# Kernel optimization log

Hardware: AMD Instinct MI355X
Metric: run time of the kernel (lower is better)

The kernel has to match this reference:

```python
import jax, jax.numpy as jnp
import numpy as np

B, T, D = 32, 512, 1024
N = 65536
H, L = 150, 17


def setup_inputs() -> dict:
    key = jax.random.key(0)
    ks = jax.random.split(key, 5)
    xs = jax.random.normal(ks[0], (B, T, D), dtype=jnp.float32)
    spans = jax.random.randint(ks[1], (N, 2), 0, T, dtype=jnp.int64 if jax.config.jax_enable_x64 else jnp.int32)
    batch_ids = jax.random.randint(ks[2], (N,), 0, B, dtype=spans.dtype)
    W1 = jax.random.normal(ks[3], (2 * D, H), dtype=jnp.float32) / np.sqrt(2 * D)
    b1 = jnp.zeros((H,), dtype=jnp.float32)
    W2 = jax.random.normal(ks[4], (H, L), dtype=jnp.float32) / np.sqrt(H)
    b2 = jnp.zeros((L,), dtype=jnp.float32)
    return {"xs": xs, "spans": spans, "batch_ids": batch_ids,
            "W1": W1, "b1": b1, "W2": W2, "b2": b2}


def reference(xs, spans, batch_ids, W1, b1, W2, b2):
    # Flatten batch/time: xs_flat [B*T, D]; offset span indices into flat space,
    # mirroring `idxs + max_length * i` in the torch forward.
    d = xs.shape[-1]
    xs_flat = xs.reshape(-1, d)
    flat_idx = spans + batch_ids[:, None] * xs.shape[1]  # [N, 2]
    # feature == 'concat': gather begin/end token reps and concat -> [N, 2D]
    feats = xs_flat[flat_idx.reshape(-1)].reshape(flat_idx.shape[0], 2 * d)
    h = jax.nn.relu(feats @ W1 + b1)  # MLP hidden layer (dropout p=0)
    scores = h @ W2 + b2              # output layer, no activation
    return scores  # [N, num_labels]; torch.split is a zero-copy view, omitted
```

## Files before the change

kernel.cpp:

```cpp
#include <hip/hip_runtime.h>
#include <stdint.h>

#define TT 512
#define DD 1024
#define NN 65536
#define HH 150
#define LL 17

typedef __bf16 bf16_t;
typedef short shortx8 __attribute__((ext_vector_type(8)));
typedef short shortx4 __attribute__((ext_vector_type(4)));
typedef float f32x4 __attribute__((ext_vector_type(4)));

typedef __attribute__((address_space(1))) const void gconst_void;
typedef __attribute__((address_space(3))) void lds_void;

static __device__ __forceinline__ short f2bf(float f) {
  return (short)__builtin_bit_cast(unsigned short, (bf16_t)f);
}
static __device__ __forceinline__ float bf2f(short s) {
  unsigned u = ((unsigned)(unsigned short)s) << 16;
  return __builtin_bit_cast(float, u);
}

__global__ __launch_bounds__(256) void prep_w(
    const float* __restrict__ W1, const float* __restrict__ W2,
    short* __restrict__ Bpp, short* __restrict__ W2p)
{
  int task = blockIdx.x * 256 + threadIdx.x;
  const int NW1 = 32 * 20 * 64;
  if (task < NW1) {
    int kb  = task / 1280;
    int rem = task - kb * 1280;
    int cb = rem >> 6, l = rem & 63;
    int cc   = cb * 16 + (l & 15);
    int half = (cc >= 160) ? 1 : 0;
    int hc   = cc - 160 * half;
    int krow = half * 1024 + kb * 32 + (l >> 4) * 8;
    shortx8 v;
#pragma unroll
    for (int j = 0; j < 8; ++j) {
      float f = (hc < HH) ? W1[(krow + j) * HH + hc] : 0.f;
      v[j] = f2bf(f);
    }
    *reinterpret_cast<shortx8*>(Bpp + task * 8) = v;
  } else if (task < NW1 + 640) {
    int t2 = task - NW1;
    int kb  = t2 >> 7;
    int rem = t2 & 127;
    int cb = rem >> 6, l = rem & 63;
    int col  = cb * 16 + (l & 15);
    int krow = kb * 32 + (l >> 4) * 8;
    shortx8 v;
#pragma unroll
    for (int j = 0; j < 8; ++j) {
      int r = krow + j;
      float f = (r < HH && col < LL) ? W2[r * LL + col] : 0.f;
      v[j] = f2bf(f);
    }
    *reinterpret_cast<shortx8*>(W2p + t2 * 8) = v;
  }
}

__global__ __launch_bounds__(512, 2) void k1_gemm(
    const float* __restrict__ xs, const short* __restrict__ Bpp,
    const float* __restrict__ b1, short* __restrict__ H)
{
  __shared__ __align__(16) char lds[81920];

  const int tid  = threadIdx.x;
  const int wv   = tid >> 6;
  const int wr   = wv >> 2;
  const int wc   = wv & 3;
  const int lane = tid & 63;
  const int l15  = lane & 15;
  const int kg   = lane >> 4;
  const int blk  = blockIdx.x;

  const char* ab[2];
#pragma unroll
  for (int rfi = 0; rfi < 2; ++rfi) {
    int row = blk * 64 + wr * 32 + rfi * 16 + l15;
    ab[rfi] = (const char*)xs + (size_t)row * 4096;
  }

  f32x4 acc[2][5];
  {
    f32x4 z = {0.f, 0.f, 0.f, 0.f};
#pragma unroll
    for (int rfi = 0; rfi < 2; ++rfi)
#pragma unroll
      for (int cbl = 0; cbl < 5; ++cbl) acc[rfi][cbl] = z;
  }

  shortx8 xbA[2][2], xbB[2][2];

#define STAGE(c, p) do { _Pragma("unroll") \
    for (int i = 0; i < 5; ++i) { \
      int f_ = wv * 5 + i;                      \
      int s_ = f_ / 20, cbb_ = f_ % 20; \
      const char* g_ = (const char*)Bpp + \
          (size_t)(((2 * (c) + s_) * 20 + cbb_) * 64 + lane) * 16; \
      char* l_ = lds + (p) * 40960 + f_ * 1024; \
      __builtin_amdgcn_global_load_lds((gconst_void*)g_, (lds_void*)l_, 16, 0, 0); \
    } \
  } while (0)

#define LOADX(c, xb) do { _Pragma("unroll") \
    for (int rfi = 0; rfi < 2; ++rfi) \
      _Pragma("unroll") \
      for (int s = 0; s < 2; ++s) { \
        int off_ = (2 * (c) + s) * 128 + kg * 32; \
        f32x4 x_ = *reinterpret_cast<const f32x4*>(ab[rfi] + off_); \
        f32x4 y_ = *reinterpret_cast<const f32x4*>(ab[rfi] + off_ + 16); \
        shortx8 t_; \
        t_[0]=f2bf(x_[0]); t_[1]=f2bf(x_[1]); t_[2]=f2bf(x_[2]); t_[3]=f2bf(x_[3]); \
        t_[4]=f2bf(y_[0]); t_[5]=f2bf(y_[1]); t_[6]=f2bf(y_[2]); t_[7]=f2bf(y_[3]); \
        xb[rfi][s] = t_; \
      } \
  } while (0)

#define COMP(p, xb) do { _Pragma("unroll") \
    for (int s = 0; s < 2; ++s) { \
      shortx8 w1f[5]; \
      _Pragma("unroll") \
      for (int cbl = 0; cbl < 5; ++cbl) \
        w1f[cbl] = *reinterpret_cast<const shortx8*>( \
            lds + (p) * 40960 + (s * 20 + wc * 5 + cbl) * 1024 + lane * 16); \
      _Pragma("unroll") \
      for (int rfi = 0; rfi < 2; ++rfi) \
        _Pragma("unroll") \
        for (int cbl = 0; cbl < 5; ++cbl) \
          acc[rfi][cbl] = __builtin_amdgcn_mfma_f32_16x16x32_bf16( \
              w1f[cbl], xb[rfi][s], acc[rfi][cbl], 0, 0, 0); \
    } \
  } while (0)

#define WAITBAR() do { \
    asm volatile("s_waitcnt vmcnt(8)" ::: "memory"); \
    __builtin_amdgcn_s_barrier(); \
    __builtin_amdgcn_sched_barrier(0); \
  } while (0)

  STAGE(0, 0);
  LOADX(0, xbA);
  WAITBAR();

  for (int cp = 0; cp < 8; ++cp) {
    int c0 = 2 * cp;
    STAGE(c0 + 1, 1);
    LOADX(c0 + 1, xbB);
    COMP(0, xbA);
    WAITBAR();
    if (cp < 7) {
      STAGE(c0 + 2, 0);
      LOADX(c0 + 2, xbA);
    }
    COMP(1, xbB);
    if (cp < 7) WAITBAR();
  }
#undef STAGE
#undef LOADX
#undef COMP
#undef WAITBAR

#pragma unroll
  for (int cbl = 0; cbl < 5; ++cbl) {
    int c0 = wc * 80 + cbl * 16 + kg * 4;
    f32x4 badd;
#pragma unroll
    for (int i = 0; i < 4; ++i)
      badd[i] = (c0 + i < HH) ? b1[c0 + i] : 0.f;
#pragma unroll
    for (int rfi = 0; rfi < 2; ++rfi) {
      f32x4 v = acc[rfi][cbl] + badd;
      shortx4 hv;
      hv[0] = f2bf(v[0]); hv[1] = f2bf(v[1]); hv[2] = f2bf(v[2]); hv[3] = f2bf(v[3]);
      int hrow = blk * 64 + wr * 32 + rfi * 16 + l15;
      *reinterpret_cast<shortx4*>(H + (size_t)hrow * 320 + c0) = hv;
    }
  }
}

__global__ __launch_bounds__(256, 4) void k2_span(
    const int* __restrict__ spans, const int* __restrict__ bids,
    const short* __restrict__ H, const short* __restrict__ W2p,
    const float* __restrict__ b2, float* __restrict__ out)
{
  const int tid  = threadIdx.x;
  const int wv   = tid >> 6;
  const int lane = tid & 63;
  const int l15  = lane & 15;
  const int kg   = lane >> 4;
  const int blk  = blockIdx.x;

  shortx8 wf[5][2];
#pragma unroll
  for (int ks = 0; ks < 5; ++ks)
#pragma unroll
    for (int cb2 = 0; cb2 < 2; ++cb2)
      wf[ks][cb2] = *reinterpret_cast<const shortx8*>(
          W2p + ((ks * 2 + cb2) * 64 + lane) * 8);

  int r  = blk * 64 + wv * 16 + l15;
  int bb = bids[r];
  int rb = bb * TT + spans[2 * r + 0];
  int re = bb * TT + spans[2 * r + 1];
  const short* pa = H + (size_t)rb * 320;
  const short* pb = H + (size_t)re * 320 + 160;

  shortx8 af[5];
#pragma unroll
  for (int ks = 0; ks < 5; ++ks) {
    shortx8 ha = *reinterpret_cast<const shortx8*>(pa + ks * 32 + kg * 8);
    shortx8 hb = *reinterpret_cast<const shortx8*>(pb + ks * 32 + kg * 8);
    shortx8 t;
#pragma unroll
    for (int j = 0; j < 8; ++j) {
      float f = bf2f(ha[j]) + bf2f(hb[j]);
      t[j] = f2bf(fmaxf(f, 0.f));
    }
    af[ks] = t;
  }

  f32x4 acc2[2];
  {
    f32x4 z = {0.f, 0.f, 0.f, 0.f};
    acc2[0] = z; acc2[1] = z;
  }
#pragma unroll
  for (int ks = 0; ks < 5; ++ks)
#pragma unroll
    for (int cb2 = 0; cb2 < 2; ++cb2)
      acc2[cb2] = __builtin_amdgcn_mfma_f32_16x16x32_bf16(
          af[ks], wf[ks][cb2], acc2[cb2], 0, 0, 0);

#pragma unroll
  for (int cb2 = 0; cb2 < 2; ++cb2) {
    int col = cb2 * 16 + l15;
    if (col < LL) {
      float bv = b2[col];
#pragma unroll
      for (int i = 0; i < 4; ++i) {
        int row = blk * 64 + wv * 16 + kg * 4 + i;
        out[(size_t)row * LL + col] = acc2[cb2][i] + bv;
      }
    }
  }
}

extern "C" void kernel_launch(void* const* d_in, const int* in_sizes, int n_in,
                              void* d_out, int out_size, void* d_ws, size_t ws_size,
                              hipStream_t stream) {
  const float* xs    = (const float*)d_in[0];
  const int*   spans = (const int*)d_in[1];
  const int*   bids  = (const int*)d_in[2];
  const float* W1    = (const float*)d_in[3];
  const float* b1    = (const float*)d_in[4];
  const float* W2    = (const float*)d_in[5];
  const float* b2    = (const float*)d_in[6];
  float* out = (float*)d_out;

  short* H   = (short*)d_ws;
  short* Bpp = H + 16384 * 320;
  short* W2p = Bpp + 327680;

  prep_w<<<163, 256, 0, stream>>>(W1, W2, Bpp, W2p);
  k1_gemm<<<256, 512, 0, stream>>>(xs, Bpp, b1, H);
  k2_span<<<1024, 256, 0, stream>>>(spans, bids, H, W2p, b2, out);
}
```

Measured before the change: 148.7 us.

## Stage activations in swizzled LDS and stream W1 fragments via registers

```diff
diff --git a/kernel.cpp b/kernel.cpp
--- a/kernel.cpp
+++ b/kernel.cpp
@@ -11,9 +11,6 @@
 typedef short shortx8 __attribute__((ext_vector_type(8)));
 typedef short shortx4 __attribute__((ext_vector_type(4)));
 typedef float f32x4 __attribute__((ext_vector_type(4)));
-
-typedef __attribute__((address_space(1))) const void gconst_void;
-typedef __attribute__((address_space(3))) void lds_void;
 
 static __device__ __forceinline__ short f2bf(float f) {
   return (short)__builtin_bit_cast(unsigned short, (bf16_t)f);
@@ -62,107 +59,116 @@
   }
 }
 
-__global__ __launch_bounds__(512, 2) void k1_gemm(
+__global__ __launch_bounds__(256, 1) void k1_gemm(
     const float* __restrict__ xs, const short* __restrict__ Bpp,
     const float* __restrict__ b1, short* __restrict__ H)
 {
-  __shared__ __align__(16) char lds[81920];
+  __shared__ __align__(16) char lds[16384];
 
   const int tid  = threadIdx.x;
-  const int wv   = tid >> 6;
-  const int wr   = wv >> 2;
-  const int wc   = wv & 3;
+  const int wc   = tid >> 6;
   const int lane = tid & 63;
   const int l15  = lane & 15;
   const int kg   = lane >> 4;
   const int blk  = blockIdx.x;
 
-  const char* ab[2];
-#pragma unroll
-  for (int rfi = 0; rfi < 2; ++rfi) {
-    int row = blk * 64 + wr * 32 + rfi * 16 + l15;
-    ab[rfi] = (const char*)xs + (size_t)row * 4096;
-  }
-
-  f32x4 acc[2][5];
+  const int arow = tid >> 2;
+  const int acol = (tid & 3) * 16;
+  const float* ag = xs + (size_t)(blk * 64 + arow) * 1024 + acol;
+  const int awb = arow * 128 + (tid & 3) * 32;
+  const int aswz_w = (arow & 7) << 4;
+  const int arb = l15 * 128 + kg * 16;
+  const int aswz_r = (l15 & 7) << 4;
+
+  const shortx8* bg = reinterpret_cast<const shortx8*>(Bpp) + (size_t)wc * 5 * 64;
+
+  f32x4 acc[4][5];
   {
     f32x4 z = {0.f, 0.f, 0.f, 0.f};
 #pragma unroll
-    for (int rfi = 0; rfi < 2; ++rfi)
-#pragma unroll
-      for (int cbl = 0; cbl < 5; ++cbl) acc[rfi][cbl] = z;
-  }
-
-  shortx8 xbA[2][2], xbB[2][2];
-
-#define STAGE(c, p) do { _Pragma("unroll") \
-    for (int i = 0; i < 5; ++i) { \
-      int f_ = wv * 5 + i;                      \
-      int s_ = f_ / 20, cbb_ = f_ % 20; \
-      const char* g_ = (const char*)Bpp + \
-          (size_t)(((2 * (c) + s_) * 20 + cbb_) * 64 + lane) * 16; \
-      char* l_ = lds + (p) * 40960 + f_ * 1024; \
-      __builtin_amdgcn_global_load_lds((gconst_void*)g_, (lds_void*)l_, 16, 0, 0); \
-    } \
-  } while (0)
-
-#define LOADX(c, xb) do { _Pragma("unroll") \
-    for (int rfi = 0; rfi < 2; ++rfi) \
-      _Pragma("unroll") \
-      for (int s = 0; s < 2; ++s) { \
-        int off_ = (2 * (c) + s) * 128 + kg * 32; \
-        f32x4 x_ = *reinterpret_cast<const f32x4*>(ab[rfi] + off_); \
-        f32x4 y_ = *reinterpret_cast<const f32x4*>(ab[rfi] + off_ + 16); \
-        shortx8 t_; \
-        t_[0]=f2bf(x_[0]); t_[1]=f2bf(x_[1]); t_[2]=f2bf(x_[2]); t_[3]=f2bf(x_[3]); \
-        t_[4]=f2bf(y_[0]); t_[5]=f2bf(y_[1]); t_[6]=f2bf(y_[2]); t_[7]=f2bf(y_[3]); \
-        xb[rfi][s] = t_; \
-      } \
-  } while (0)
-
-#define COMP(p, xb) do { _Pragma("unroll") \
-    for (int s = 0; s < 2; ++s) { \
-      shortx8 w1f[5]; \
+    for (int rf = 0; rf < 4; ++rf)
+#pragma unroll
+      for (int cbl = 0; cbl < 5; ++cbl) acc[rf][cbl] = z;
+  }
+
+  f32x4 aregA[4], aregB[4];
+  shortx8 bregA[10], bregB[10];
+
+#define GLOAD_A(reg, c) do { _Pragma("unroll") \
+    for (int i = 0; i < 4; ++i) \
+      reg[i] = *reinterpret_cast<const f32x4*>(ag + (c) * 64 + i * 4); \
+  } while (0)
+
+#define GLOAD_B(reg, c) do { _Pragma("unroll") \
+    for (int s = 0; s < 2; ++s) \
       _Pragma("unroll") \
       for (int cbl = 0; cbl < 5; ++cbl) \
-        w1f[cbl] = *reinterpret_cast<const shortx8*>( \
-            lds + (p) * 40960 + (s * 20 + wc * 5 + cbl) * 1024 + lane * 16); \
+        reg[s * 5 + cbl] = bg[(size_t)((2 * (c) + s) * 20 + cbl) * 64 + lane]; \
+  } while (0)
+
+#define WRITE_A(reg, p) do { \
+    shortx8 lo_, hi_; \
+    _Pragma("unroll") \
+    for (int i = 0; i < 8; ++i) { \
+      lo_[i] = f2bf(reg[i >> 2][i & 3]); \
+      hi_[i] = f2bf(reg[2 + (i >> 2)][i & 3]); \
+    } \
+    char* b_ = lds + (p) * 8192; \
+    *reinterpret_cast<shortx8*>(b_ + ((awb +  0) ^ aswz_w)) = lo_; \
+    *reinterpret_cast<shortx8*>(b_ + ((awb + 16) ^ aswz_w)) = hi_; \
+  } while (0)
+
+#define COMP(breg, p) do { \
+    const char* b_ = lds + (p) * 8192; \
+    _Pragma("unroll") \
+    for (int s = 0; s < 2; ++s) { \
+      shortx8 af_[4]; \
       _Pragma("unroll") \
-      for (int rfi = 0; rfi < 2; ++rfi) \
+      for (int rf = 0; rf < 4; ++rf) \
+        af_[rf] = *reinterpret_cast<const shortx8*>( \
+            b_ + ((arb + rf * 2048 + s * 64) ^ aswz_r)); \
+      _Pragma("unroll") \
+      for (int rf = 0; rf < 4; ++rf) \
         _Pragma("unroll") \
         for (int cbl = 0; cbl < 5; ++cbl) \
-          acc[rfi][cbl] = __builtin_amdgcn_mfma_f32_16x16x32_bf16( \
-              w1f[cbl], xb[rfi][s], acc[rfi][cbl], 0, 0, 0); \
+          acc[rf][cbl] = __builtin_amdgcn_mfma_f32_16x16x32_bf16( \
+              breg[s * 5 + cbl], af_[rf], acc[rf][cbl], 0, 0, 0); \
     } \
   } while (0)
 
-#define WAITBAR() do { \
-    asm volatile("s_waitcnt vmcnt(8)" ::: "memory"); \
+#define BAR() do { \
+    asm volatile("s_waitcnt lgkmcnt(0)" ::: "memory"); \
     __builtin_amdgcn_s_barrier(); \
     __builtin_amdgcn_sched_barrier(0); \
   } while (0)
 
-  STAGE(0, 0);
-  LOADX(0, xbA);
-  WAITBAR();
-
+  GLOAD_A(aregA, 0);
+  WRITE_A(aregA, 0);
+  GLOAD_B(bregA, 0);
+  GLOAD_A(aregB, 1);
+  BAR();
+
+#pragma unroll 1
   for (int cp = 0; cp < 8; ++cp) {
     int c0 = 2 * cp;
-    STAGE(c0 + 1, 1);
-    LOADX(c0 + 1, xbB);
-    COMP(0, xbA);
-    WAITBAR();
-    if (cp < 7) {
-      STAGE(c0 + 2, 0);
-      LOADX(c0 + 2, xbA);
-    }
-    COMP(1, xbB);
-    if (cp < 7) WAITBAR();
-  }
-#undef STAGE
-#undef LOADX
+    GLOAD_B(bregB, c0 + 1);
+    COMP(bregA, 0);
+    WRITE_A(aregB, 1);
+    if (c0 + 2 < 16) GLOAD_A(aregA, c0 + 2);
+    BAR();
+    if (c0 + 2 < 16) GLOAD_B(bregA, c0 + 2);
+    COMP(bregB, 1);
+    if (c0 + 2 < 16) {
+      WRITE_A(aregA, 0);
+      if (c0 + 3 < 16) GLOAD_A(aregB, c0 + 3);
+      BAR();
+    }
+  }
+#undef GLOAD_A
+#undef GLOAD_B
+#undef WRITE_A
 #undef COMP
-#undef WAITBAR
+#undef BAR
 
 #pragma unroll
   for (int cbl = 0; cbl < 5; ++cbl) {
@@ -172,11 +178,11 @@
     for (int i = 0; i < 4; ++i)
       badd[i] = (c0 + i < HH) ? b1[c0 + i] : 0.f;
 #pragma unroll
-    for (int rfi = 0; rfi < 2; ++rfi) {
-      f32x4 v = acc[rfi][cbl] + badd;
+    for (int rf = 0; rf < 4; ++rf) {
+      f32x4 v = acc[rf][cbl] + badd;
       shortx4 hv;
       hv[0] = f2bf(v[0]); hv[1] = f2bf(v[1]); hv[2] = f2bf(v[2]); hv[3] = f2bf(v[3]);
-      int hrow = blk * 64 + wr * 32 + rfi * 16 + l15;
+      int hrow = blk * 64 + rf * 16 + l15;
       *reinterpret_cast<shortx4*>(H + (size_t)hrow * 320 + c0) = hv;
     }
   }
@@ -266,6 +272,6 @@
   short* W2p = Bpp + 327680;
 
   prep_w<<<163, 256, 0, stream>>>(W1, W2, Bpp, W2p);
-  k1_gemm<<<256, 512, 0, stream>>>(xs, Bpp, b1, H);
+  k1_gemm<<<256, 256, 0, stream>>>(xs, Bpp, b1, H);
   k2_span<<<1024, 256, 0, stream>>>(spans, bids, H, W2p, b2, out);
 }
```

Result: faster. 135.2 us (-9.1%).
